# Kernel tuning notes

Hardware: AMD Instinct MI355X
Metric: run time of the kernel (lower is better)

## Reference

```python
import jax, jax.numpy as jnp
import numpy as np

BREAKING_TOKENS = jnp.array([13], dtype=jnp.int64)
NUM_HEADS = 16

B, S, E = 2, 2048, 1024


def setup_inputs() -> dict:
    key = jax.random.key(0)
    k1, k2, k3, k4, k5, k6 = jax.random.split(key, 6)
    scale = 1.0 / np.sqrt(E)
    return {
        "input_embeddings": jax.random.normal(k1, (B, S, E), dtype=jnp.float32),
        "token_ids": jax.random.randint(k2, (B, S), 0, 100, dtype=jnp.int64),
        "in_proj_weight": jax.random.normal(k3, (3 * E, E), dtype=jnp.float32) * scale,
        "in_proj_bias": jax.random.normal(k4, (3 * E,), dtype=jnp.float32) * 0.02,
        "out_proj_weight": jax.random.normal(k5, (E, E), dtype=jnp.float32) * scale,
        "out_proj_bias": jax.random.normal(k6, (E,), dtype=jnp.float32) * 0.02,
    }


def _sentence_mask(token_ids):
    # Faithful vectorization of the triple Python loop:
    # mask[b, i, j] is True iff j <= i and no breaking token occurs at positions j..i.
    brk = jnp.isin(token_ids, BREAKING_TOKENS)            # [B, S] bool
    s = jnp.cumsum(brk.astype(jnp.int32), axis=-1)        # inclusive cumsum of breaks
    s_prev = s - brk.astype(jnp.int32)                    # cumsum up to j-1
    seq = token_ids.shape[-1]
    causal = jnp.tril(jnp.ones((seq, seq), dtype=bool))   # j <= i
    # no break in [j, i]  <=>  s[i] == s_prev[j]
    return causal[None, :, :] & (s[:, :, None] == s_prev[:, None, :])  # [B, S, S]


def reference(input_embeddings, token_ids, in_proj_weight, in_proj_bias,
              out_proj_weight, out_proj_bias):
    x = input_embeddings
    b, s, e = x.shape
    h = NUM_HEADS
    d = e // h

    # torch bool attn_mask semantics: True = NOT allowed to attend (-inf).
    mask_true = _sentence_mask(token_ids)                 # [B, S, S]

    qkv = x @ in_proj_weight.T + in_proj_bias             # [B, S, 3E]
    q, k, v = jnp.split(qkv, 3, axis=-1)
    q = q.reshape(b, s, h, d)
    k = k.reshape(b, s, h, d)
    v = v.reshape(b, s, h, d)

    scores = jnp.einsum("bqhd,bkhd->bhqk", q, k) / jnp.sqrt(jnp.asarray(d, x.dtype))
    scores = jnp.where(mask_true[:, None, :, :], -jnp.inf, scores)
    attn = jax.nn.softmax(scores, axis=-1)                # [B, H, S, S]

    out = jnp.einsum("bhqk,bkhd->bqhd", attn, v).reshape(b, s, e)
    return out @ out_proj_weight.T + out_proj_bias
```

## Files before the change

kernel.cpp:

```cpp
#include <hip/hip_runtime.h>
#include <math.h>
#include <stdint.h>

#define BB 2
#define SS 2048
#define EE 1024
#define HH 16
#define DD 64
#define E3 3072
#define NR (BB*SS)
#define QKW 2048
#define NSPLIT 2
#define QB 128

#define C2Q 0.18033688011112042f

typedef __attribute__((ext_vector_type(8))) short short8;
typedef __attribute__((ext_vector_type(4))) float f32x4;
typedef __attribute__((ext_vector_type(4))) uint uint4v;

__device__ __forceinline__ ushort f2bf(float f) {
    uint u = __float_as_uint(f);
    uint r = u + 0x7FFFu + ((u >> 16) & 1u);
    return (ushort)(r >> 16);
}
__device__ __forceinline__ short8 pack8(float4 a, float4 b) {
    short8 v;
    v[0] = (short)f2bf(a.x); v[1] = (short)f2bf(a.y); v[2] = (short)f2bf(a.z); v[3] = (short)f2bf(a.w);
    v[4] = (short)f2bf(b.x); v[5] = (short)f2bf(b.y); v[6] = (short)f2bf(b.z); v[7] = (short)f2bf(b.w);
    return v;
}
__device__ __forceinline__ uint cvtpk(float lo, float hi) {
    uint d;
    asm("v_cvt_pk_bf16_f32 %0, %1, %2" : "=v"(d) : "v"(lo), "v"(hi));
    return d;
}
__device__ __forceinline__ float vexp2(float x) {
    float r;
    asm("v_exp_f32 %0, %1" : "=v"(r) : "v"(x));
    return r;
}

__global__ __launch_bounds__(256) void cvt_all(const float* __restrict__ x,
                                               const float* __restrict__ win,
                                               const float* __restrict__ wout,
                                               ushort* __restrict__ xb,
                                               ushort* __restrict__ winb,
                                               ushort* __restrict__ woutb) {
    const int NX = NR * EE / 8, NW = E3 * EE / 8;
    int i = blockIdx.x * 256 + threadIdx.x;
    const float* src; ushort* dst; int j;
    if (i < NX)           { src = x;    dst = xb;    j = i; }
    else if (i < NX + NW) { src = win;  dst = winb;  j = i - NX; }
    else                  { src = wout; dst = woutb; j = i - NX - NW; }
    const float4* p = (const float4*)src + (size_t)j * 2;
    float4 a = p[0], b = p[1];
    *((short8*)dst + j) = pack8(a, b);
}

__global__ void scan_kernel(const int* __restrict__ tok, int* __restrict__ lbrk) {
    int b = blockIdx.x;
    int t = threadIdx.x;
    __shared__ int pmax[256];
    int loc[8];
    int base = b * SS + t * 8;
    int lm = -1;
#pragma unroll
    for (int i = 0; i < 8; i++) {
        if (tok[base + i] == 13) lm = t * 8 + i;
        loc[i] = lm;
    }
    pmax[t] = lm;
    __syncthreads();
    if (t == 0) {
        int acc = -1;
        for (int i = 0; i < 256; i++) { int tmp = pmax[i]; pmax[i] = acc; acc = max(acc, tmp); }
    }
    __syncthreads();
    int off = pmax[t];
#pragma unroll
    for (int i = 0; i < 8; i++)
        lbrk[base + i] = max(off, loc[i]);
}

template<int OUT_BF16>
__global__ __launch_bounds__(256) void gemm_mfma(const ushort* __restrict__ A,
                                                 const ushort* __restrict__ Bw,
                                                 const float* __restrict__ bias,
                                                 void* __restrict__ Cv,
                                                 ushort* __restrict__ vTp,
                                                 int strideC, int K) {
    __shared__ ushort As[2][128 * 32];
    __shared__ ushort Bs[2][128 * 32];
    int id = blockIdx.y * gridDim.x + blockIdx.x;
    {
        int cpx = (gridDim.x * gridDim.y) >> 3;
        id = (id & 7) * cpx + (id >> 3);
    }
    const int bm = (id % gridDim.x) * 128;
    const int bn = (id / gridDim.x) * 128;
    const int tid = threadIdx.x;
    const int w = tid >> 6, lane = tid & 63;
    const int l16 = lane & 15, lk = lane >> 4;
    const int wr = w >> 1, wc = w & 1;

    f32x4 acc[4][4];
#pragma unroll
    for (int mi = 0; mi < 4; mi++)
#pragma unroll
        for (int ni = 0; ni < 4; ni++)
            acc[mi][ni] = (f32x4){0.f, 0.f, 0.f, 0.f};

    const int ci  = w * 2;
    const int rA0 = lane >> 2;
    const int gsh = (lane & 3) ^ ((lane >> 2) & 3);

#define GSTAGE(buf, k0)                                                                      \
    {                                                                                        \
        _Pragma("unroll") for (int i2 = 0; i2 < 2; ++i2) {                                   \
            int c = ci + i2;                                                                 \
            int r = c * 16 + rA0;                                                            \
            const ushort* ga = A + (size_t)(bn + r) * K + (k0) + gsh * 8;                    \
            const ushort* gb = Bw + (size_t)(bm + r) * K + (k0) + gsh * 8;                   \
            __builtin_amdgcn_global_load_lds(                                                \
                (const __attribute__((address_space(1))) void*)ga,                           \
                (__attribute__((address_space(3))) void*)((char*)&As[buf][0] + c * 1024),    \
                16, 0, 0);                                                                   \
            __builtin_amdgcn_global_load_lds(                                                \
                (const __attribute__((address_space(1))) void*)gb,                           \
                (__attribute__((address_space(3))) void*)((char*)&Bs[buf][0] + c * 1024),    \
                16, 0, 0);                                                                   \
        }                                                                                    \
    }

    const int pp = (lk ^ (l16 & 3)) * 8;
    const int NT = K / 32;

    GSTAGE(0, 0);
    __syncthreads();

    for (int t = 0; t < NT; ++t) {
        int cur = t & 1;
        if (t + 1 < NT) GSTAGE(cur ^ 1, (t + 1) * 32);
        const ushort* Ab = &As[cur][0];
        const ushort* Bb = &Bs[cur][0];
        short8 af[4], bfr[4];
#pragma unroll
        for (int mi = 0; mi < 4; ++mi) {
            int r = wr * 64 + mi * 16 + l16;
            af[mi] = *(const short8*)(Ab + r * 32 + pp);
        }
#pragma unroll
        for (int ni = 0; ni < 4; ++ni) {
            int r = wc * 64 + ni * 16 + l16;
            bfr[ni] = *(const short8*)(Bb + r * 32 + pp);
        }
#pragma unroll
        for (int mi = 0; mi < 4; ++mi)
#pragma unroll
            for (int ni = 0; ni < 4; ++ni)
                acc[mi][ni] = __builtin_amdgcn_mfma_f32_16x16x32_bf16(af[mi], bfr[ni], acc[mi][ni], 0, 0, 0);
        __syncthreads();
    }
#undef GSTAGE

#pragma unroll
    for (int ni = 0; ni < 4; ++ni) {
        int col = bm + wc * 64 + ni * 16 + l16;
        float bv = bias[col];
        const bool isV = OUT_BF16 && (col >= 2 * EE);
#pragma unroll
        for (int mi = 0; mi < 4; ++mi) {
            int row = bn + wr * 64 + mi * 16 + lk * 4;
            if (isV) {
                int d   = col - 2 * EE;
                int bb2 = row >> 11;
                int tok = row & 2047;
                int c0  = (tok & ~31) | (lk << 3) | ((mi & 1) << 2);
                uint2 pk;
                pk.x = cvtpk(acc[mi][ni][0] + bv, acc[mi][ni][1] + bv);
                pk.y = cvtpk(acc[mi][ni][2] + bv, acc[mi][ni][3] + bv);
                *(uint2*)(vTp + ((size_t)(bb2 * HH + (d >> 6)) * DD + (d & 63)) * SS + c0) = pk;
            } else {
#pragma unroll
                for (int j = 0; j < 4; ++j) {
                    float vv = acc[mi][ni][j] + bv;
                    if (OUT_BF16 && col < EE) vv *= C2Q;
                    if (OUT_BF16)
                        ((ushort*)Cv)[(size_t)(row + j) * strideC + col] = f2bf(vv);
                    else
                        ((float*)Cv)[(size_t)(row + j) * strideC + col] = vv;
                }
            }
        }
    }
}

__global__ __launch_bounds__(256, 2) void attn_mfma(const ushort* __restrict__ qk,
                                                    const ushort* __restrict__ vT,
                                                    const int* __restrict__ lbrk,
                                                    ushort* __restrict__ po,
                                                    float* __restrict__ pl) {
    __shared__ ushort ks[2][64 * 64];
    __shared__ ushort vt[2][64 * 64];

    int bid = (blockIdx.x & 7) * 128 + (blockIdx.x >> 3);
    const int kq = bid & 1;
    const int qb = (bid >> 1) & 15;
    const int h  = (bid >> 5) & 15;
    const int b  = bid >> 9;
    const int q0b = qb * QB;
    const int T0 = kq * 16;
    const int NTT = 16;
    const int tid = threadIdx.x;
    const int w = tid >> 6, lane = tid & 63;
    const int l16 = lane & 15, lk = lane >> 4;
    const int q0w = q0b + w * 32;

    const ushort* qk_b  = qk + (size_t)(b * SS) * QKW;
    const ushort* vT_bh = vT + ((size_t)(b * HH + h)) * DD * SS;

    short8 qf[2][2];
#pragma unroll
    for (int qg = 0; qg < 2; qg++)
#pragma unroll
        for (int kk = 0; kk < 2; kk++)
            qf[qg][kk] = *(const short8*)(qk_b + (size_t)(q0w + qg * 16 + l16) * QKW + h * DD + kk * 32 + lk * 8);

    int lb1[2]; uint wid[2];
#pragma unroll
    for (int qg = 0; qg < 2; qg++) {
        int q = q0w + qg * 16 + l16;
        int lb = lbrk[b * SS + q];
        lb1[qg] = lb + 1;
        wid[qg] = (uint)(q - lb);
    }

    const int srow = lane >> 3;
    const int slot = lane & 7;
    const ushort* gK[2];
    const ushort* gV[2];
#pragma unroll
    for (int i = 0; i < 2; i++) {
        int r = w * 16 + i * 8 + srow;
        int sl = (slot ^ (r & 7)) << 3;
        gK[i] = qk_b + (size_t)r * QKW + EE + h * DD + sl;
        gV[i] = vT_bh + (size_t)r * SS + sl;
    }

#define STAGE(buf, kt)                                                                            \
    {                                                                                             \
        _Pragma("unroll") for (int i = 0; i < 2; ++i) {                                           \
            __builtin_amdgcn_global_load_lds(                                                     \
                (const __attribute__((address_space(1))) void*)(gK[i] + (size_t)(kt) * 64 * QKW), \
                (__attribute__((address_space(3))) void*)((char*)&ks[buf][0] + w * 2048 + i * 1024), \
                16, 0, 0);                                                                        \
            __builtin_amdgcn_global_load_lds(                                                     \
                (const __attribute__((address_space(1))) void*)(gV[i] + (size_t)(kt) * 64),       \
                (__attribute__((address_space(3))) void*)((char*)&vt[buf][0] + w * 2048 + i * 1024), \
                16, 0, 0);                                                                        \
        }                                                                                         \
    }

    const int xr = l16 & 7;
    int perm[2];
#pragma unroll
    for (int u = 0; u < 2; u++) perm[u] = ((u * 4 + lk) ^ xr) << 3;

    short8 ones8;
#pragma unroll
    for (int i = 0; i < 8; i++) ones8[i] = (short)0x3F80;

    f32x4 o[4][2];
    f32x4 l_acc[2];
#pragma unroll
    for (int dg = 0; dg < 4; dg++)
#pragma unroll
        for (int qg = 0; qg < 2; qg++)
            o[dg][qg] = (f32x4){0.f, 0.f, 0.f, 0.f};
#pragma unroll
    for (int qg = 0; qg < 2; qg++) l_acc[qg] = (f32x4){0.f, 0.f, 0.f, 0.f};

    const int tmask = qb * 2 + 1;

    STAGE(0, T0);
    STAGE(1, T0 + 1);

    for (int t = 0; t < NTT; ++t) {
        if (t < NTT - 1) asm volatile("s_waitcnt vmcnt(4)" ::: "memory");
        else             asm volatile("s_waitcnt vmcnt(0)" ::: "memory");
        __builtin_amdgcn_s_barrier();

        const int T = T0 + t;
        const ushort* kb = &ks[t & 1][0];
        const ushort* vb = &vt[t & 1][0];
        const bool domask = (T <= tmask);

#pragma unroll
        for (int t32 = 0; t32 < 2; ++t32) {
            uint pu[2][4];
#pragma unroll
            for (int hi = 0; hi < 2; ++hi) {
                const int jg = t32 * 2 + hi;
                short8 kf0 = *(const short8*)(kb + (jg * 16 + l16) * 64 + perm[0]);
                short8 kf1 = *(const short8*)(kb + (jg * 16 + l16) * 64 + perm[1]);
                f32x4 s[2];
#pragma unroll
                for (int qg = 0; qg < 2; qg++) {
                    s[qg] = (f32x4){0.f, 0.f, 0.f, 0.f};
                    s[qg] = __builtin_amdgcn_mfma_f32_16x16x32_bf16(kf0, qf[qg][0], s[qg], 0, 0, 0);
                    s[qg] = __builtin_amdgcn_mfma_f32_16x16x32_bf16(kf1, qf[qg][1], s[qg], 0, 0, 0);
                }
                const int jbase = T * 64 + t32 * 32 + hi * 16 + lk * 4;
#pragma unroll
                for (int qg = 0; qg < 2; qg++) {
                    float p0, p1, p2, p3;
                    if (domask) {
                        int jb = jbase - lb1[qg];
                        p0 = vexp2((uint)(jb + 0) < wid[qg] ? -1e30f : s[qg][0]);
                        p1 = vexp2((uint)(jb + 1) < wid[qg] ? -1e30f : s[qg][1]);
                        p2 = vexp2((uint)(jb + 2) < wid[qg] ? -1e30f : s[qg][2]);
                        p3 = vexp2((uint)(jb + 3) < wid[qg] ? -1e30f : s[qg][3]);
                    } else {
                        p0 = vexp2(s[qg][0]);
                        p1 = vexp2(s[qg][1]);
                        p2 = vexp2(s[qg][2]);
                        p3 = vexp2(s[qg][3]);
                    }
                    pu[qg][hi * 2]     = cvtpk(p0, p1);
                    pu[qg][hi * 2 + 1] = cvtpk(p2, p3);
                }
            }
            short8 pfB[2];
#pragma unroll
            for (int qg = 0; qg < 2; qg++) {
                uint4v u;
                u[0] = pu[qg][0]; u[1] = pu[qg][1]; u[2] = pu[qg][2]; u[3] = pu[qg][3];
                pfB[qg] = __builtin_bit_cast(short8, u);
            }
#pragma unroll
            for (int qg = 0; qg < 2; qg++)
                l_acc[qg] = __builtin_amdgcn_mfma_f32_16x16x32_bf16(ones8, pfB[qg], l_acc[qg], 0, 0, 0);
#pragma unroll
            for (int dg = 0; dg < 4; dg++) {
                short8 vf = *(const short8*)(vb + (dg * 16 + l16) * 64 + perm[t32]);
#pragma unroll
                for (int qg = 0; qg < 2; qg++)
                    o[dg][qg] = __builtin_amdgcn_mfma_f32_16x16x32_bf16(vf, pfB[qg], o[dg][qg], 0, 0, 0);
            }
        }

        asm volatile("s_waitcnt lgkmcnt(0)" ::: "memory");
        __builtin_amdgcn_s_barrier();
        if (t + 2 < NTT) STAGE(t & 1, T0 + t + 2);
    }
#undef STAGE

    ushort* po_k = po + (size_t)kq * NR * EE;
#pragma unroll
    for (int qg = 0; qg < 2; qg++) {
        int qo = q0w + qg * 16 + l16;
        ushort* dst = po_k + (size_t)(b * SS + qo) * EE + h * DD + lk * 4;
#pragma unroll
        for (int dg = 0; dg < 4; dg++) {
            uint u0 = cvtpk(o[dg][qg][0], o[dg][qg][1]);
            uint u1 = cvtpk(o[dg][qg][2], o[dg][qg][3]);
            uint2 pk; pk.x = u0; pk.y = u1;
            *(uint2*)(dst + dg * 16) = pk;
        }
        if (lk == 0)
            pl[((size_t)(kq * BB + b) * HH + h) * SS + qo] = l_acc[qg][0];
    }
}

__global__ __launch_bounds__(256) void combine(const ushort* __restrict__ po,
                                               const float* __restrict__ pl,
                                               ushort* __restrict__ aob) {
    int i8 = blockIdx.x * 256 + threadIdx.x;
    const int bq = i8 >> 7;
    const int h  = (i8 >> 3) & 15;
    const int b  = bq >> 11;
    const int q  = bq & 2047;
    float lsum = 0.f;
#pragma unroll
    for (int k = 0; k < NSPLIT; k++)
        lsum += pl[((size_t)(k * BB + b) * HH + h) * SS + q];
    float inv = 1.f / lsum;
    float accv[8] = {0.f};
#pragma unroll
    for (int k = 0; k < NSPLIT; k++) {
        short8 a = *((const short8*)(po + (size_t)k * NR * EE) + i8);
#pragma unroll
        for (int j = 0; j < 8; j++)
            accv[j] += __uint_as_float(((uint)(ushort)a[j]) << 16);
    }
    short8 r;
#pragma unroll
    for (int j = 0; j < 8; j++)
        r[j] = (short)f2bf(accv[j] * inv);
    *((short8*)aob + i8) = r;
}

extern "C" void kernel_launch(void* const* d_in, const int* in_sizes, int n_in,
                              void* d_out, int out_size, void* d_ws, size_t ws_size,
                              hipStream_t stream) {
    const float* x    = (const float*)d_in[0];
    const int*   tok  = (const int*)d_in[1];
    const float* win  = (const float*)d_in[2];
    const float* bin  = (const float*)d_in[3];
    const float* wout = (const float*)d_in[4];
    const float* bout = (const float*)d_in[5];
    float* out = (float*)d_out;

    ushort* xb    = (ushort*)d_ws;
    ushort* woutb = xb + (size_t)NR * EE;
    ushort* qkb   = woutb + (size_t)EE * EE;
    ushort* vTb   = qkb + (size_t)NR * QKW;
    float*  pl    = (float*)(vTb + (size_t)BB * HH * DD * SS);
    int*    lbrk  = (int*)(pl + (size_t)NSPLIT * BB * HH * SS);
    ushort* winb  = (ushort*)(lbrk + NR);
    ushort* po    = winb;
    ushort* aob   = xb;

    int ncvt = (NR * EE + E3 * EE + EE * EE) / 8;
    cvt_all<<<ncvt / 256, 256, 0, stream>>>(x, win, wout, xb, winb, woutb);

    scan_kernel<<<BB, 256, 0, stream>>>(tok, lbrk);

    gemm_mfma<1><<<dim3(E3 / 128, NR / 128), 256, 0, stream>>>(xb, winb, bin, (void*)qkb, vTb, QKW, EE);

    attn_mfma<<<BB * HH * (SS / QB) * NSPLIT, 256, 0, stream>>>(qkb, vTb, lbrk, po, pl);

    combine<<<NR * EE / 8 / 256, 256, 0, stream>>>(po, pl, aob);

    gemm_mfma<0><<<dim3(EE / 128, NR / 128), 256, 0, stream>>>(aob, woutb, bout, (void*)out, nullptr, EE, EE);
}
```

Baseline: 127.7 us.

## Fuse split-KV combine into output projection GEMM and merge scan into convert

Removes the separate combine kernel by having the output-projection GEMM load both split-KV partial outputs and partial softmax sums, normalize them in registers, and write bf16 into LDS as the A tile. The token scan kernel is also folded into the conversion kernel as extra blocks, cutting two launches. This avoids writing and re-reading the combined attention output buffer, at the cost of register-staged (non-async) A loads and duplicated normalization work across N-column blocks.

```diff
diff --git a/kernel.cpp b/kernel.cpp
--- a/kernel.cpp
+++ b/kernel.cpp
@@ -40,15 +40,47 @@
     asm("v_exp_f32 %0, %1" : "=v"(r) : "v"(x));
     return r;
 }
-
-__global__ __launch_bounds__(256) void cvt_all(const float* __restrict__ x,
-                                               const float* __restrict__ win,
-                                               const float* __restrict__ wout,
-                                               ushort* __restrict__ xb,
-                                               ushort* __restrict__ winb,
-                                               ushort* __restrict__ woutb) {
-    const int NX = NR * EE / 8, NW = E3 * EE / 8;
-    int i = blockIdx.x * 256 + threadIdx.x;
+__device__ __forceinline__ float bf2f(short s) {
+    return __uint_as_float(((uint)(ushort)s) << 16);
+}
+
+__global__ __launch_bounds__(256) void cvt_scan(const float* __restrict__ x,
+                                                const float* __restrict__ win,
+                                                const float* __restrict__ wout,
+                                                ushort* __restrict__ xb,
+                                                ushort* __restrict__ winb,
+                                                ushort* __restrict__ woutb,
+                                                const int* __restrict__ tok,
+                                                int* __restrict__ lbrk) {
+    const int NX = NR * EE / 8, NW = E3 * EE / 8, NWO = EE * EE / 8;
+    const int NCVT = (NX + NW + NWO) / 256;
+    __shared__ int pmax[256];
+    int blk = blockIdx.x;
+    int t = threadIdx.x;
+    if (blk >= NCVT) {
+        int b = blk - NCVT;
+        int loc[8];
+        int base = b * SS + t * 8;
+        int lm = -1;
+#pragma unroll
+        for (int i = 0; i < 8; i++) {
+            if (tok[base + i] == 13) lm = t * 8 + i;
+            loc[i] = lm;
+        }
+        pmax[t] = lm;
+        __syncthreads();
+        if (t == 0) {
+            int acc = -1;
+            for (int i = 0; i < 256; i++) { int tmp = pmax[i]; pmax[i] = acc; acc = max(acc, tmp); }
+        }
+        __syncthreads();
+        int off = pmax[t];
+#pragma unroll
+        for (int i = 0; i < 8; i++)
+            lbrk[base + i] = max(off, loc[i]);
+        return;
+    }
+    int i = blk * 256 + t;
     const float* src; ushort* dst; int j;
     if (i < NX)           { src = x;    dst = xb;    j = i; }
     else if (i < NX + NW) { src = win;  dst = winb;  j = i - NX; }
@@ -56,31 +88,6 @@
     const float4* p = (const float4*)src + (size_t)j * 2;
     float4 a = p[0], b = p[1];
     *((short8*)dst + j) = pack8(a, b);
-}
-
-__global__ void scan_kernel(const int* __restrict__ tok, int* __restrict__ lbrk) {
-    int b = blockIdx.x;
-    int t = threadIdx.x;
-    __shared__ int pmax[256];
-    int loc[8];
-    int base = b * SS + t * 8;
-    int lm = -1;
-#pragma unroll
-    for (int i = 0; i < 8; i++) {
-        if (tok[base + i] == 13) lm = t * 8 + i;
-        loc[i] = lm;
-    }
-    pmax[t] = lm;
-    __syncthreads();
-    if (t == 0) {
-        int acc = -1;
-        for (int i = 0; i < 256; i++) { int tmp = pmax[i]; pmax[i] = acc; acc = max(acc, tmp); }
-    }
-    __syncthreads();
-    int off = pmax[t];
-#pragma unroll
-    for (int i = 0; i < 8; i++)
-        lbrk[base + i] = max(off, loc[i]);
 }
 
 template<int OUT_BF16>
@@ -192,6 +199,139 @@
                         ((float*)Cv)[(size_t)(row + j) * strideC + col] = vv;
                 }
             }
+        }
+    }
+}
+
+__global__ __launch_bounds__(256) void gemm_out(const ushort* __restrict__ po,
+                                                const float* __restrict__ pl,
+                                                const ushort* __restrict__ Bw,
+                                                const float* __restrict__ bias,
+                                                float* __restrict__ C) {
+    __shared__ ushort As[2][128 * 32];
+    __shared__ ushort Bs[2][128 * 32];
+    int id = blockIdx.y * gridDim.x + blockIdx.x;
+    {
+        int cpx = (gridDim.x * gridDim.y) >> 3;
+        id = (id & 7) * cpx + (id >> 3);
+    }
+    const int bm = (id % gridDim.x) * 128;
+    const int bn = (id / gridDim.x) * 128;
+    const int K = EE;
+    const int tid = threadIdx.x;
+    const int w = tid >> 6, lane = tid & 63;
+    const int l16 = lane & 15, lk = lane >> 4;
+    const int wr = w >> 1, wc = w & 1;
+
+    f32x4 acc[4][4];
+#pragma unroll
+    for (int mi = 0; mi < 4; mi++)
+#pragma unroll
+        for (int ni = 0; ni < 4; ni++)
+            acc[mi][ni] = (f32x4){0.f, 0.f, 0.f, 0.f};
+
+    const int ci  = w * 2;
+    const int rA0 = lane >> 2;
+    const int gsh = (lane & 3) ^ ((lane >> 2) & 3);
+
+    const ushort* p0 = po;
+    const ushort* p1 = po + (size_t)NR * EE;
+    int rg[2], bq_b[2], bq_q[2];
+#pragma unroll
+    for (int i2 = 0; i2 < 2; ++i2) {
+        rg[i2]   = bn + (ci + i2) * 16 + rA0;
+        bq_b[i2] = rg[i2] >> 11;
+        bq_q[i2] = rg[i2] & 2047;
+    }
+
+    short8 a0[2], a1[2];
+    float  lv0[2], lv1[2];
+
+#define ALOAD(k0)                                                                            \
+    {                                                                                        \
+        int h = (k0) >> 6;                                                                   \
+        _Pragma("unroll") for (int i2 = 0; i2 < 2; ++i2) {                                   \
+            const size_t off = (size_t)rg[i2] * EE + (k0) + gsh * 8;                         \
+            a0[i2] = *(const short8*)(p0 + off);                                             \
+            a1[i2] = *(const short8*)(p1 + off);                                             \
+            lv0[i2] = pl[((size_t)(0 * BB + bq_b[i2]) * HH + h) * SS + bq_q[i2]];            \
+            lv1[i2] = pl[((size_t)(1 * BB + bq_b[i2]) * HH + h) * SS + bq_q[i2]];            \
+        }                                                                                    \
+    }
+
+#define AWRITE(buf)                                                                          \
+    {                                                                                        \
+        _Pragma("unroll") for (int i2 = 0; i2 < 2; ++i2) {                                   \
+            float inv = 1.f / (lv0[i2] + lv1[i2]);                                           \
+            uint4v u;                                                                        \
+            _Pragma("unroll") for (int j = 0; j < 4; ++j) {                                  \
+                float flo = (bf2f(a0[i2][2 * j])     + bf2f(a1[i2][2 * j]))     * inv;       \
+                float fhi = (bf2f(a0[i2][2 * j + 1]) + bf2f(a1[i2][2 * j + 1])) * inv;       \
+                u[j] = cvtpk(flo, fhi);                                                      \
+            }                                                                                \
+            *(uint4v*)&As[buf][(ci + i2) * 512 + lane * 8] = u;                              \
+        }                                                                                    \
+    }
+
+#define BSTAGE(buf, k0)                                                                      \
+    {                                                                                        \
+        _Pragma("unroll") for (int i2 = 0; i2 < 2; ++i2) {                                   \
+            int c = ci + i2;                                                                 \
+            int r = c * 16 + rA0;                                                            \
+            const ushort* gb = Bw + (size_t)(bm + r) * K + (k0) + gsh * 8;                   \
+            __builtin_amdgcn_global_load_lds(                                                \
+                (const __attribute__((address_space(1))) void*)gb,                           \
+                (__attribute__((address_space(3))) void*)((char*)&Bs[buf][0] + c * 1024),    \
+                16, 0, 0);                                                                   \
+        }                                                                                    \
+    }
+
+    const int pp = (lk ^ (l16 & 3)) * 8;
+    const int NT = K / 32;
+
+    ALOAD(0);
+    BSTAGE(0, 0);
+    AWRITE(0);
+    __syncthreads();
+
+    for (int t = 0; t < NT; ++t) {
+        int cur = t & 1;
+        if (t + 1 < NT) { ALOAD((t + 1) * 32); BSTAGE(cur ^ 1, (t + 1) * 32); }
+        const ushort* Ab = &As[cur][0];
+        const ushort* Bb = &Bs[cur][0];
+        short8 af[4], bfr[4];
+#pragma unroll
+        for (int mi = 0; mi < 4; ++mi) {
+            int r = wr * 64 + mi * 16 + l16;
+            af[mi] = *(const short8*)(Ab + r * 32 + pp);
+        }
+#pragma unroll
+        for (int ni = 0; ni < 4; ++ni) {
+            int r = wc * 64 + ni * 16 + l16;
+            bfr[ni] = *(const short8*)(Bb + r * 32 + pp);
+        }
+#pragma unroll
+        for (int mi = 0; mi < 4; ++mi)
+#pragma unroll
+            for (int ni = 0; ni < 4; ++ni)
+                acc[mi][ni] = __builtin_amdgcn_mfma_f32_16x16x32_bf16(af[mi], bfr[ni], acc[mi][ni], 0, 0, 0);
+        if (t + 1 < NT) AWRITE(cur ^ 1);
+        __syncthreads();
+    }
+#undef ALOAD
+#undef AWRITE
+#undef BSTAGE
+
+#pragma unroll
+    for (int ni = 0; ni < 4; ++ni) {
+        int col = bm + wc * 64 + ni * 16 + l16;
+        float bv = bias[col];
+#pragma unroll
+        for (int mi = 0; mi < 4; ++mi) {
+            int row = bn + wr * 64 + mi * 16 + lk * 4;
+#pragma unroll
+            for (int j = 0; j < 4; ++j)
+                C[(size_t)(row + j) * EE + col] = acc[mi][ni][j] + bv;
         }
     }
 }
@@ -373,34 +513,6 @@
     }
 }
 
-__global__ __launch_bounds__(256) void combine(const ushort* __restrict__ po,
-                                               const float* __restrict__ pl,
-                                               ushort* __restrict__ aob) {
-    int i8 = blockIdx.x * 256 + threadIdx.x;
-    const int bq = i8 >> 7;
-    const int h  = (i8 >> 3) & 15;
-    const int b  = bq >> 11;
-    const int q  = bq & 2047;
-    float lsum = 0.f;
-#pragma unroll
-    for (int k = 0; k < NSPLIT; k++)
-        lsum += pl[((size_t)(k * BB + b) * HH + h) * SS + q];
-    float inv = 1.f / lsum;
-    float accv[8] = {0.f};
-#pragma unroll
-    for (int k = 0; k < NSPLIT; k++) {
-        short8 a = *((const short8*)(po + (size_t)k * NR * EE) + i8);
-#pragma unroll
-        for (int j = 0; j < 8; j++)
-            accv[j] += __uint_as_float(((uint)(ushort)a[j]) << 16);
-    }
-    short8 r;
-#pragma unroll
-    for (int j = 0; j < 8; j++)
-        r[j] = (short)f2bf(accv[j] * inv);
-    *((short8*)aob + i8) = r;
-}
-
 extern "C" void kernel_launch(void* const* d_in, const int* in_sizes, int n_in,
                               void* d_out, int out_size, void* d_ws, size_t ws_size,
                               hipStream_t stream) {
@@ -420,18 +532,13 @@
     int*    lbrk  = (int*)(pl + (size_t)NSPLIT * BB * HH * SS);
     ushort* winb  = (ushort*)(lbrk + NR);
     ushort* po    = winb;
-    ushort* aob   = xb;
-
-    int ncvt = (NR * EE + E3 * EE + EE * EE) / 8;
-    cvt_all<<<ncvt / 256, 256, 0, stream>>>(x, win, wout, xb, winb, woutb);
-
-    scan_kernel<<<BB, 256, 0, stream>>>(tok, lbrk);
+
+    int ncvt = (NR * EE + E3 * EE + EE * EE) / 8 / 256;
+    cvt_scan<<<ncvt + BB, 256, 0, stream>>>(x, win, wout, xb, winb, woutb, tok, lbrk);
 
     gemm_mfma<1><<<dim3(E3 / 128, NR / 128), 256, 0, stream>>>(xb, winb, bin, (void*)qkb, vTb, QKW, EE);
 
     attn_mfma<<<BB * HH * (SS / QB) * NSPLIT, 256, 0, stream>>>(qkb, vTb, lbrk, po, pl);
 
-    combine<<<NR * EE / 8 / 256, 256, 0, stream>>>(po, pl, aob);
-
-    gemm_mfma<0><<<dim3(EE / 128, NR / 128), 256, 0, stream>>>(aob, woutb, bout, (void*)out, nullptr, EE, EE);
-}
+    gemm_out<<<dim3(EE / 128, NR / 128), 256, 0, stream>>>(po, pl, woutb, bout, out);
+}
```

After: 133.8 us. +4.8%, slower.
